# Performance work log

Measured on AMD Instinct MI355X. Metric: run time of the kernel, lower is better.

The kernel has to match this reference:

```python
import jax, jax.numpy as jnp
import numpy as np

B, S = 512, 1024          # batch sentences x tokens
VOCAB = 100000            # word alphabet size
CHAR_LEN = 32             # chars per word in lut
CHAR_VOCAB = 60           # char alphabet size
N_POS = 40                # POS tag set size
MAX_CANDS = 4000          # padded per-POS candidate list length
N_PRIV = 8                # first N_PRIV tags are privacy terms (e.g. NNP-like)
CTX_RATE = 0.15           # cfg.ctx_obf_rate
PRI_RATE = 1.0            # cfg.pri_obf_rate


def setup_inputs() -> dict:
    key = jax.random.key(0)
    ks = jax.random.split(key, 8)
    inp_word = jax.random.randint(ks[0], (B, S), 0, VOCAB, dtype=jnp.int32)
    inp_char = jax.random.randint(ks[1], (B, S, CHAR_LEN), 0, CHAR_VOCAB, dtype=jnp.int32)
    inp_pos = jax.random.randint(ks[2], (B, S), 0, N_POS, dtype=jnp.int32)
    inp_mask = jax.random.randint(ks[3], (B, S), 0, 2, dtype=jnp.int32)
    ctx_rand = jax.random.uniform(ks[4], (B, S), dtype=jnp.float32)
    pri_rand = jax.random.uniform(ks[5], (B, S), dtype=jnp.float32)
    cand_u = jax.random.uniform(ks[6], (B, S), dtype=jnp.float32)
    kl, kt, kc = jax.random.split(ks[7], 3)
    lut = jax.random.randint(kl, (VOCAB, CHAR_LEN), 0, CHAR_VOCAB, dtype=jnp.int32)
    tgt_table = jax.random.randint(kt, (N_POS, MAX_CANDS), 0, VOCAB, dtype=jnp.int32)
    counts = jax.random.randint(kc, (N_POS,), 1, MAX_CANDS, dtype=jnp.int32)
    priv_pos = jnp.arange(N_POS) < N_PRIV  # bool [N_POS]
    return {"inp_word": inp_word, "inp_char": inp_char, "inp_pos": inp_pos,
            "inp_mask": inp_mask, "ctx_rand": ctx_rand, "pri_rand": pri_rand,
            "cand_u": cand_u, "lut": lut, "tgt_table": tgt_table,
            "counts": counts, "priv_pos": priv_pos}


def reference(inp_word, inp_char, inp_pos, inp_mask, ctx_rand, pri_rand, cand_u,
              lut, tgt_table, counts, priv_pos):
    # pri_mask: union of pos_mask over privacy POS tags
    pri_mask = priv_pos[inp_pos]                      # bool [B,S]
    # Bernoulli obfuscation masks (torch.rand(shape) < rate)
    ctx_obf = ctx_rand < CTX_RATE                     # bool [B,S]
    pri_obf = pri_rand < PRI_RATE                     # bool [B,S]
    # per-token obf decision: privacy tags use pri_obf, context tags use ctx_obf
    obf_mask = jnp.where(pri_mask, pri_obf, ctx_obf)  # bool [B,S]
    # uniform random candidate from the token's POS candidate list
    cnt = counts[inp_pos]                             # int32 [B,S]
    idx = jnp.minimum((cand_u * cnt.astype(cand_u.dtype)).astype(jnp.int32),
                      cnt - 1)                        # [B,S] in [0, cnt)
    cdt = tgt_table[inp_pos, idx]                     # int32 [B,S]
    obf_word = jnp.where(obf_mask, cdt, inp_word)     # masked_scatter_ equivalent
    obf_char = lut[obf_word]                          # word_to_char gather [B,S,CHAR_LEN]
    cpy_mask = inp_mask.astype(bool) & (inp_word == obf_word)
    return (obf_word, inp_word, obf_char, inp_pos, obf_mask, pri_mask, cpy_mask)
```

## Files before the change

kernel.cpp:

```cpp
#include <hip/hip_runtime.h>

#define B_DIM 512
#define S_DIM 1024
#define NTOK (B_DIM * S_DIM)
#define CHAR_LEN 32
#define MAX_CANDS 4000
#define N_PRIV 8
#define CTX_RATE 0.15f

typedef int vint4 __attribute__((ext_vector_type(4)));


__device__ __forceinline__ void do_token(
    int token, int sub,
    const int* __restrict__ inp_word,
    const int* __restrict__ inp_pos,
    const int* __restrict__ inp_mask,
    const float* __restrict__ ctx_rand,
    const float* __restrict__ pri_rand,
    const float* __restrict__ cand_u,
    const vint4* __restrict__ lut4,
    const int* __restrict__ tgt_table,
    const int* __restrict__ counts,
    int* __restrict__ out)
{
    int pos   = __builtin_nontemporal_load(&inp_pos[token]);
    int word  = __builtin_nontemporal_load(&inp_word[token]);
    float cr  = __builtin_nontemporal_load(&ctx_rand[token]);
    float pr  = __builtin_nontemporal_load(&pri_rand[token]);
    float cu  = __builtin_nontemporal_load(&cand_u[token]);

    bool pri_mask = (pos < N_PRIV);
    bool obf = pri_mask ? (pr < 1.0f) : (cr < CTX_RATE);

    int cnt = counts[pos];
    int idx = (int)(cu * (float)cnt);
    idx = min(idx, cnt - 1);
    int cdt = tgt_table[pos * MAX_CANDS + idx];
    int obf_word = obf ? cdt : word;

    vint4 v = lut4[obf_word * 8 + sub];
    vint4* out_char4 = (vint4*)(out + (size_t)NTOK * 2);
    __builtin_nontemporal_store(v, &out_char4[(size_t)token * 8 + sub]);

    if (sub == 0) {
        __builtin_nontemporal_store(obf_word, &out[token]);
        __builtin_nontemporal_store(word, &out[NTOK + token]);
        __builtin_nontemporal_store(pos, &out[(size_t)NTOK * 34 + token]);
        __builtin_nontemporal_store(obf ? 1 : 0, &out[(size_t)NTOK * 35 + token]);
        __builtin_nontemporal_store(pri_mask ? 1 : 0, &out[(size_t)NTOK * 36 + token]);
        int msk = __builtin_nontemporal_load(&inp_mask[token]);
        bool cpy = (msk != 0) && (word == obf_word);
        __builtin_nontemporal_store(cpy ? 1 : 0, &out[(size_t)NTOK * 37 + token]);
    }
}

__global__ __launch_bounds__(256) void alltag_kernel(
    const int* __restrict__ inp_word,
    const int* __restrict__ inp_pos,
    const int* __restrict__ inp_mask,
    const float* __restrict__ ctx_rand,
    const float* __restrict__ pri_rand,
    const float* __restrict__ cand_u,
    const vint4* __restrict__ lut4,
    const int* __restrict__ tgt_table,
    const int* __restrict__ counts,
    int* __restrict__ out)
{
    int g = blockIdx.x * blockDim.x + threadIdx.x;
    int token0 = g >> 3;
    int sub    = g & 7;
    int token1 = token0 + (NTOK / 2);

    do_token(token0, sub, inp_word, inp_pos, inp_mask, ctx_rand, pri_rand,
             cand_u, lut4, tgt_table, counts, out);
    do_token(token1, sub, inp_word, inp_pos, inp_mask, ctx_rand, pri_rand,
             cand_u, lut4, tgt_table, counts, out);
}

extern "C" void kernel_launch(void* const* d_in, const int* in_sizes, int n_in,
                              void* d_out, int out_size, void* d_ws, size_t ws_size,
                              hipStream_t stream) {
    const int*   inp_word  = (const int*)  d_in[0];
    const int*   inp_pos   = (const int*)  d_in[2];
    const int*   inp_mask  = (const int*)  d_in[3];
    const float* ctx_rand  = (const float*)d_in[4];
    const float* pri_rand  = (const float*)d_in[5];
    const float* cand_u    = (const float*)d_in[6];
    const vint4* lut4      = (const vint4*)d_in[7];
    const int*   tgt_table = (const int*)  d_in[8];
    const int*   counts    = (const int*)  d_in[9];
    int* out = (int*)d_out;

    const int total = NTOK * 4;
    const int block = 256;
    const int grid  = (total + block - 1) / block;
    alltag_kernel<<<grid, block, 0, stream>>>(inp_word, inp_pos, inp_mask,
                                              ctx_rand, pri_rand, cand_u,
                                              lut4, tgt_table, counts, out);
}
```

Baseline: 172.7 us.

## Compute per-token scalars once per thread and stage words in shared memory for lut gather

New measurement: 158.9 us (median of 2 runs). -8.0%, faster.

```diff
diff --git a/kernel.cpp b/kernel.cpp
--- a/kernel.cpp
+++ b/kernel.cpp
@@ -11,50 +11,6 @@
 typedef int vint4 __attribute__((ext_vector_type(4)));
 
 
-__device__ __forceinline__ void do_token(
-    int token, int sub,
-    const int* __restrict__ inp_word,
-    const int* __restrict__ inp_pos,
-    const int* __restrict__ inp_mask,
-    const float* __restrict__ ctx_rand,
-    const float* __restrict__ pri_rand,
-    const float* __restrict__ cand_u,
-    const vint4* __restrict__ lut4,
-    const int* __restrict__ tgt_table,
-    const int* __restrict__ counts,
-    int* __restrict__ out)
-{
-    int pos   = __builtin_nontemporal_load(&inp_pos[token]);
-    int word  = __builtin_nontemporal_load(&inp_word[token]);
-    float cr  = __builtin_nontemporal_load(&ctx_rand[token]);
-    float pr  = __builtin_nontemporal_load(&pri_rand[token]);
-    float cu  = __builtin_nontemporal_load(&cand_u[token]);
-
-    bool pri_mask = (pos < N_PRIV);
-    bool obf = pri_mask ? (pr < 1.0f) : (cr < CTX_RATE);
-
-    int cnt = counts[pos];
-    int idx = (int)(cu * (float)cnt);
-    idx = min(idx, cnt - 1);
-    int cdt = tgt_table[pos * MAX_CANDS + idx];
-    int obf_word = obf ? cdt : word;
-
-    vint4 v = lut4[obf_word * 8 + sub];
-    vint4* out_char4 = (vint4*)(out + (size_t)NTOK * 2);
-    __builtin_nontemporal_store(v, &out_char4[(size_t)token * 8 + sub]);
-
-    if (sub == 0) {
-        __builtin_nontemporal_store(obf_word, &out[token]);
-        __builtin_nontemporal_store(word, &out[NTOK + token]);
-        __builtin_nontemporal_store(pos, &out[(size_t)NTOK * 34 + token]);
-        __builtin_nontemporal_store(obf ? 1 : 0, &out[(size_t)NTOK * 35 + token]);
-        __builtin_nontemporal_store(pri_mask ? 1 : 0, &out[(size_t)NTOK * 36 + token]);
-        int msk = __builtin_nontemporal_load(&inp_mask[token]);
-        bool cpy = (msk != 0) && (word == obf_word);
-        __builtin_nontemporal_store(cpy ? 1 : 0, &out[(size_t)NTOK * 37 + token]);
-    }
-}
-
 __global__ __launch_bounds__(256) void alltag_kernel(
     const int* __restrict__ inp_word,
     const int* __restrict__ inp_pos,
@@ -67,15 +23,56 @@
     const int* __restrict__ counts,
     int* __restrict__ out)
 {
-    int g = blockIdx.x * blockDim.x + threadIdx.x;
-    int token0 = g >> 3;
-    int sub    = g & 7;
-    int token1 = token0 + (NTOK / 2);
+    __shared__ int s_obf_word[256];
 
-    do_token(token0, sub, inp_word, inp_pos, inp_mask, ctx_rand, pri_rand,
-             cand_u, lut4, tgt_table, counts, out);
-    do_token(token1, sub, inp_word, inp_pos, inp_mask, ctx_rand, pri_rand,
-             cand_u, lut4, tgt_table, counts, out);
+    const int tid        = threadIdx.x;
+    const int token_base = blockIdx.x * 256;
+
+    {
+        const int token = token_base + tid;
+        int   pos  = __builtin_nontemporal_load(&inp_pos[token]);
+        int   word = __builtin_nontemporal_load(&inp_word[token]);
+        float cr   = __builtin_nontemporal_load(&ctx_rand[token]);
+        float pr   = __builtin_nontemporal_load(&pri_rand[token]);
+        float cu   = __builtin_nontemporal_load(&cand_u[token]);
+        int   msk  = __builtin_nontemporal_load(&inp_mask[token]);
+
+        bool pri_mask = (pos < N_PRIV);
+        bool obf = pri_mask ? (pr < 1.0f) : (cr < CTX_RATE);
+
+        int cnt = counts[pos];
+        int idx = (int)(cu * (float)cnt);
+        idx = min(idx, cnt - 1);
+        int cdt = tgt_table[pos * MAX_CANDS + idx];
+        int obf_word = obf ? cdt : word;
+
+        s_obf_word[tid] = obf_word;
+
+        __builtin_nontemporal_store(obf_word, &out[token]);
+        __builtin_nontemporal_store(word, &out[NTOK + token]);
+        __builtin_nontemporal_store(pos, &out[(size_t)NTOK * 34 + token]);
+        __builtin_nontemporal_store(obf ? 1 : 0, &out[(size_t)NTOK * 35 + token]);
+        __builtin_nontemporal_store(pri_mask ? 1 : 0, &out[(size_t)NTOK * 36 + token]);
+        bool cpy = (msk != 0) && (word == obf_word);
+        __builtin_nontemporal_store(cpy ? 1 : 0, &out[(size_t)NTOK * 37 + token]);
+    }
+
+    __syncthreads();
+
+    {
+        const int sub   = tid & 7;
+        const int group = tid >> 3;
+        vint4* out_char4 = (vint4*)(out + (size_t)NTOK * 2);
+
+#pragma unroll
+        for (int i = 0; i < 8; ++i) {
+            int lt = group + 32 * i;
+            int w  = s_obf_word[lt];
+            vint4 v = lut4[w * 8 + sub];
+            __builtin_nontemporal_store(
+                v, &out_char4[(size_t)(token_base + lt) * 8 + sub]);
+        }
+    }
 }
 
 extern "C" void kernel_launch(void* const* d_in, const int* in_sizes, int n_in,
@@ -92,9 +89,8 @@
     const int*   counts    = (const int*)  d_in[9];
     int* out = (int*)d_out;
 
-    const int total = NTOK * 4;
     const int block = 256;
-    const int grid  = (total + block - 1) / block;
+    const int grid  = NTOK / block;
     alltag_kernel<<<grid, block, 0, stream>>>(inp_word, inp_pos, inp_mask,
                                               ctx_rand, pri_rand, cand_u,
                                               lut4, tgt_table, counts, out);
```
